# Kernel tuning notes

Measured on AMD Instinct MI355X. Metric: run time of the kernel, lower is better.

## Reference

```python
import jax, jax.numpy as jnp
import numpy as np

N_NODES = 50000
N_EDGES = 300000
HEADS = 2
OUT_CH = 128
BN_EPS = 1e-5
NEG_SLOPE = 0.2


def _batchnorm(x, g, b):
    # training-mode BatchNorm1d: biased batch statistics
    mean = x.mean(axis=0)
    var = x.var(axis=0)
    return (x - mean) * jax.lax.rsqrt(var + BN_EPS) * g + b


def _gatv2(x, src, dst, edge_attr, Wl, bl, Wr, br, We, att, bias, concat):
    # PyG GATv2Conv, share_weights=False, aggr='add'
    n = x.shape[0]
    xl = (x @ Wl + bl).reshape(n, HEADS, OUT_CH)  # source messages
    xr = (x @ Wr + br).reshape(n, HEADS, OUT_CH)  # destination term
    ee = (edge_attr @ We).reshape(-1, HEADS, OUT_CH)
    s = jax.nn.leaky_relu(xl[src] + xr[dst] + ee, NEG_SLOPE)  # [E,H,C]
    alpha = jnp.einsum('ehc,hc->eh', s, att)  # [E,H]
    # segment softmax over edges grouped by destination node
    m = jax.ops.segment_max(alpha, dst, num_segments=n)
    a = jnp.exp(alpha - m[dst])
    den = jax.ops.segment_sum(a, dst, num_segments=n)
    a = a / (den[dst] + 1e-16)
    out = jax.ops.segment_sum(xl[src] * a[:, :, None], dst, num_segments=n)  # [N,H,C]
    out = out.reshape(n, HEADS * OUT_CH) if concat else out.mean(axis=1)
    return out + bias


def setup_inputs() -> dict:
    key = jax.random.key(0)
    ks = jax.random.split(key, 16)
    d = {}
    d['h'] = jax.random.normal(ks[0], (N_NODES, 5), jnp.float32)
    d['edge_index'] = jax.random.randint(ks[1], (2, N_EDGES), 0, N_NODES, jnp.int64)
    d['edge_weight'] = jax.random.uniform(ks[2], (N_EDGES, 1), jnp.float32)
    d['bn0_g'] = jnp.ones((5,), jnp.float32)
    d['bn0_b'] = jnp.zeros((5,), jnp.float32)
    d['bn1_g'] = jnp.ones((256,), jnp.float32)
    d['bn1_b'] = jnp.zeros((256,), jnp.float32)
    def lin(k, fan_in, fan_out):
        return jax.random.normal(k, (fan_in, fan_out), jnp.float32) * (1.0 / np.sqrt(fan_in))
    # conv1: in=5 -> heads*out=256, concat=True
    d['c1_Wl'] = lin(ks[3], 5, 256); d['c1_bl'] = jnp.zeros((256,), jnp.float32)
    d['c1_Wr'] = lin(ks[4], 5, 256); d['c1_br'] = jnp.zeros((256,), jnp.float32)
    d['c1_We'] = lin(ks[5], 1, 256)
    d['c1_att'] = jax.random.normal(ks[6], (HEADS, OUT_CH), jnp.float32) * 0.1
    d['c1_bias'] = jnp.zeros((256,), jnp.float32)
    # mu: in=256 -> 128, concat=False
    d['mu_Wl'] = lin(ks[7], 256, 256); d['mu_bl'] = jnp.zeros((256,), jnp.float32)
    d['mu_Wr'] = lin(ks[8], 256, 256); d['mu_br'] = jnp.zeros((256,), jnp.float32)
    d['mu_We'] = lin(ks[9], 1, 256)
    d['mu_att'] = jax.random.normal(ks[10], (HEADS, OUT_CH), jnp.float32) * 0.1
    d['mu_bias'] = jnp.zeros((128,), jnp.float32)
    # log_std: same shapes as mu
    d['ls_Wl'] = lin(ks[11], 256, 256); d['ls_bl'] = jnp.zeros((256,), jnp.float32)
    d['ls_Wr'] = lin(ks[12], 256, 256); d['ls_br'] = jnp.zeros((256,), jnp.float32)
    d['ls_We'] = lin(ks[13], 1, 256)
    d['ls_att'] = jax.random.normal(ks[14], (HEADS, OUT_CH), jnp.float32) * 0.1
    d['ls_bias'] = jnp.zeros((128,), jnp.float32)
    return d


def reference(h, edge_index, edge_weight, bn0_g, bn0_b, bn1_g, bn1_b,
              c1_Wl, c1_bl, c1_Wr, c1_br, c1_We, c1_att, c1_bias,
              mu_Wl, mu_bl, mu_Wr, mu_br, mu_We, mu_att, mu_bias,
              ls_Wl, ls_bl, ls_Wr, ls_br, ls_We, ls_att, ls_bias):
    src, dst = edge_index[0], edge_index[1]
    x = _batchnorm(h, bn0_g, bn0_b)
    x = _gatv2(x, src, dst, edge_weight, c1_Wl, c1_bl, c1_Wr, c1_br, c1_We, c1_att, c1_bias, concat=True)
    x = jax.nn.relu(_batchnorm(x, bn1_g, bn1_b))
    # dropout identity (eval / deterministic)
    mu = _gatv2(x, src, dst, edge_weight, mu_Wl, mu_bl, mu_Wr, mu_br, mu_We, mu_att, mu_bias, concat=False)
    log_std = _gatv2(x, src, dst, edge_weight, ls_Wl, ls_bl, ls_Wr, ls_br, ls_We, ls_att, ls_bias, concat=False)
    return (mu, log_std)
```

## Files before the change

### kernel.cpp

```cpp
#include <hip/hip_runtime.h>
#include <math.h>

#define N_NODES 50000
#define N_EDGES 300000
#define BN_EPS 1e-5f
#define NEG_SLOPE 0.2f

#define RB_COUNT 3128
#define SCAN_TILES 49
#define BN1_BLOCKS 523
#define K5_BLOCKS 1024

#define AGG_BLOCKS 2048
#define AGG_STRIDE (AGG_BLOCKS * 4)

#define PREP_BN0 128
#define PREP_EC  1172
#define PREP_PW  128

typedef short bf8v __attribute__((ext_vector_type(8)));
typedef float f4v __attribute__((ext_vector_type(4)));
typedef float f2v __attribute__((ext_vector_type(2)));

__device__ inline unsigned short f2bf(float f) {
    union { float f; unsigned u; } c; c.f = f;
    unsigned r = c.u + 0x7fffu + ((c.u >> 16) & 1u);
    return (unsigned short)(r >> 16);
}

__device__ inline unsigned f2bf2(float lo, float hi) {
    return (unsigned)f2bf(lo) | ((unsigned)f2bf(hi) << 16);
}

__device__ inline f2v bfpair(unsigned u) {
    union { unsigned u; float f; } lo, hi;
    lo.u = u << 16;
    hi.u = u & 0xffff0000u;
    f2v r; r.x = lo.f; r.y = hi.f;
    return r;
}

__device__ inline void async_copy16(void* lds, const void* g) {
    __builtin_amdgcn_global_load_lds(
        (const __attribute__((address_space(1))) unsigned int*)g,
        (__attribute__((address_space(3))) unsigned int*)lds, 16, 0, 0);
}

__global__ __launch_bounds__(256) void prep(
        const float* __restrict__ h, float* __restrict__ acc,
        const int* __restrict__ dst, int* __restrict__ count,
        const float* __restrict__ Wl0, const float* __restrict__ Wr0,
        const float* __restrict__ Wl1, const float* __restrict__ Wr1,
        unsigned short* __restrict__ bp) {
    int b = blockIdx.x;
    if (b < PREP_BN0) {
        __shared__ float lds[4][10];
        int tid = threadIdx.x;
        int lane = tid & 63, wave = tid >> 6;
        float ls[5] = {0,0,0,0,0}, lq[5] = {0,0,0,0,0};
        for (int r = b * 256 + tid; r < N_NODES; r += PREP_BN0 * 256) {
            #pragma unroll
            for (int k = 0; k < 5; k++) {
                float v = h[r*5 + k];
                ls[k] += v; lq[k] += v*v;
            }
        }
        #pragma unroll
        for (int k = 0; k < 5; k++) {
            #pragma unroll
            for (int m = 1; m <= 32; m <<= 1) {
                ls[k] += __shfl_xor(ls[k], m, 64);
                lq[k] += __shfl_xor(lq[k], m, 64);
            }
        }
        if (lane == 0) {
            #pragma unroll
            for (int k = 0; k < 5; k++) { lds[wave][k] = ls[k]; lds[wave][5+k] = lq[k]; }
        }
        __syncthreads();
        if (tid < 10) {
            float s = lds[0][tid] + lds[1][tid] + lds[2][tid] + lds[3][tid];
            atomicAdd(&acc[tid], s);
        }
    } else if (b < PREP_BN0 + PREP_EC) {
        int e = (b - PREP_BN0) * 256 + threadIdx.x;
        if (e < N_EDGES) atomicAdd(&count[dst[e]], 1);
    } else {
        int t = (b - PREP_BN0 - PREP_EC) * 256 + threadIdx.x;
        int lane = t & 63;
        int nt = (t >> 6) & 31;
        int kc = (t >> 11) & 7;
        int conv = t >> 14;
        int col = nt * 16 + (lane & 15);
        int k0 = kc * 32 + (lane >> 4) * 8;
        const float* W = conv ? (col < 256 ? Wl1 : Wr1) : (col < 256 ? Wl0 : Wr0);
        int c = col & 255;
        union { unsigned short h[8]; uint4 u; } tmp;
        #pragma unroll
        for (int j = 0; j < 8; j++) tmp.h[j] = f2bf(W[(size_t)(k0 + j) * 256 + c]);
        *reinterpret_cast<uint4*>(bp + (size_t)t * 8) = tmp.u;
    }
}

__global__ void local_scan(const int* __restrict__ count, int* __restrict__ offsets,
                           int* __restrict__ tileSum) {
    __shared__ int wsum[16];
    int tid = threadIdx.x;
    int lane = tid & 63, wv = tid >> 6;
    int i = blockIdx.x * 1024 + tid;
    int v = (i < N_NODES) ? count[i] : 0;
    int inc = v;
    #pragma unroll
    for (int off = 1; off < 64; off <<= 1) {
        int t = __shfl_up(inc, off, 64);
        if (lane >= off) inc += t;
    }
    if (lane == 63) wsum[wv] = inc;
    __syncthreads();
    if (wv == 0) {
        int val = (lane < 16) ? wsum[lane] : 0;
        int inc2 = val;
        #pragma unroll
        for (int off = 1; off < 16; off <<= 1) {
            int t = __shfl_up(inc2, off, 64);
            if (lane >= off) inc2 += t;
        }
        if (lane < 16) wsum[lane] = inc2 - val;
    }
    __syncthreads();
    int excl = inc - v + wsum[wv];
    if (i < N_NODES) offsets[i] = excl;
    if (tid == 1023) tileSum[blockIdx.x] = excl + v;
}

__global__ void add_prefix(int* __restrict__ offsets, const int* __restrict__ tileSum,
                           int* __restrict__ cursor) {
    __shared__ int spref;
    int tid = threadIdx.x;
    if (tid < 64) {
        int v = (tid < blockIdx.x) ? tileSum[tid] : 0;
        #pragma unroll
        for (int m = 1; m <= 32; m <<= 1) v += __shfl_xor(v, m, 64);
        if (tid == 0) spref = v;
    }
    __syncthreads();
    int i = blockIdx.x * 1024 + tid;
    if (i < N_NODES) {
        int o = offsets[i] + spref;
        offsets[i] = o;
        cursor[i] = o;
    }
    if (blockIdx.x == 0 && tid == 0) offsets[N_NODES] = N_EDGES;
}

__global__ void edge_scatter(const int* __restrict__ dst, const int* __restrict__ src,
                             const float* __restrict__ ew, int* __restrict__ cursor,
                             int2* __restrict__ sep) {
    int e = blockIdx.x * blockDim.x + threadIdx.x;
    if (e < N_EDGES) {
        int pos = atomicAdd(&cursor[dst[e]], 1);
        sep[pos] = make_int2(src[e], __float_as_int(ew[e]));
    }
}

__global__ __launch_bounds__(128) void gemm_k5(const float* __restrict__ h,
        const float* __restrict__ acc10, const float* __restrict__ g5,
        const float* __restrict__ b5,
        const float* __restrict__ Wl, const float* __restrict__ bl,
        const float* __restrict__ Wr, const float* __restrict__ br,
        unsigned short* __restrict__ xl, unsigned short* __restrict__ xr) {
    int c = threadIdx.x * 2;
    float sc[5], sh[5];
    #pragma unroll
    for (int k = 0; k < 5; k++) {
        float mean = acc10[k] * (1.f / N_NODES);
        float var  = acc10[5 + k] * (1.f / N_NODES) - mean * mean;
        float s = g5[k] * rsqrtf(var + BN_EPS);
        sc[k] = s; sh[k] = b5[k] - mean * s;
    }
    float wl0[5], wl1[5], wr0[5], wr1[5];
    #pragma unroll
    for (int k = 0; k < 5; k++) {
        wl0[k] = Wl[k*256 + c]; wl1[k] = Wl[k*256 + c + 1];
        wr0[k] = Wr[k*256 + c]; wr1[k] = Wr[k*256 + c + 1];
    }
    float bl0 = bl[c], bl1 = bl[c+1], br0 = br[c], br1 = br[c+1];
    int n = blockIdx.x;
    float hv[5];
    if (n < N_NODES) {
        #pragma unroll
        for (int k = 0; k < 5; k++) hv[k] = h[n*5 + k];
    }
    for (; n < N_NODES; n += K5_BLOCKS) {
        int n2 = n + K5_BLOCKS;
        float hn[5] = {0,0,0,0,0};
        if (n2 < N_NODES) {
            #pragma unroll
            for (int k = 0; k < 5; k++) hn[k] = h[n2*5 + k];
        }
        float l0 = bl0, l1 = bl1, r0 = br0, r1 = br1;
        #pragma unroll
        for (int k = 0; k < 5; k++) {
            float a = hv[k] * sc[k] + sh[k];
            l0 += a * wl0[k]; l1 += a * wl1[k];
            r0 += a * wr0[k]; r1 += a * wr1[k];
        }
        *reinterpret_cast<unsigned*>(xl + (size_t)n*256 + c) = f2bf2(l0, l1);
        *reinterpret_cast<unsigned*>(xr + (size_t)n*256 + c) = f2bf2(r0, r1);
        #pragma unroll
        for (int k = 0; k < 5; k++) hv[k] = hn[k];
    }
}

__global__ __launch_bounds__(256) void gemm_mfma(const unsigned short* __restrict__ xh,
        const float* __restrict__ ss1,
        const unsigned short* __restrict__ bp,
        const float* __restrict__ bl0, const float* __restrict__ br0,
        const float* __restrict__ bl1, const float* __restrict__ br1,
        unsigned short* __restrict__ xlA, unsigned short* __restrict__ xrA,
        unsigned short* __restrict__ xlB, unsigned short* __restrict__ xrB) {
    __shared__ unsigned short Bs[2][16][512];
    int b = blockIdx.x;
    int cv = b >= 1564; b -= cv * 1564;
    int h  = b >= 782;  b -= h * 782;
    int lane = threadIdx.x & 63;
    int wave = threadIdx.x >> 6;
    int rb = b * 4 + wave;

    const unsigned short* bsrc = bp + (size_t)cv * 131072 + (size_t)h * 8192 + lane * 8;
    auto stage = [&](int buf, int kc) {
        #pragma unroll
        for (int j = 0; j < 4; j++) {
            int f = wave * 4 + j;
            async_copy16(&Bs[buf][f][lane * 8], bsrc + (size_t)kc * 16384 + f * 512);
        }
    };
    stage(0, 0);

    int row = rb * 16 + (lane & 15);
    int k0b = (lane >> 4) * 8;
    bool rok = row < N_NODES;
    bf8v a[8];
    #pragma unroll
    for (int kc = 0; kc < 8; kc++) {
        int k0 = kc * 32 + k0b;
        union { unsigned short hh[8]; uint4 u; bf8v v; } tmp;
        if (rok) {
            uint4 u = *(const uint4*)(xh + (size_t)row * 256 + k0);
            f4v s0 = *(const f4v*)(ss1 + k0);
            f4v s1 = *(const f4v*)(ss1 + k0 + 4);
            f4v h0 = *(const f4v*)(ss1 + 256 + k0);
            f4v h1 = *(const f4v*)(ss1 + 256 + k0 + 4);
            float f[8];
            f2v p;
            p = bfpair(u.x); f[0] = p.x; f[1] = p.y;
            p = bfpair(u.y); f[2] = p.x; f[3] = p.y;
            p = bfpair(u.z); f[4] = p.x; f[5] = p.y;
            p = bfpair(u.w); f[6] = p.x; f[7] = p.y;
            float scv[8] = {s0.x, s0.y, s0.z, s0.w, s1.x, s1.y, s1.z, s1.w};
            float shv[8] = {h0.x, h0.y, h0.z, h0.w, h1.x, h1.y, h1.z, h1.w};
            #pragma unroll
            for (int j = 0; j < 8; j++) {
                float v = f[j] * scv[j] + shv[j];
                v = v > 0.f ? v : 0.f;
                tmp.hh[j] = f2bf(v);
            }
        } else {
            tmp.u = (uint4){0u, 0u, 0u, 0u};
        }
        a[kc] = tmp.v;
    }

    f4v acc[16];
    #pragma unroll
    for (int t = 0; t < 16; t++) acc[t] = (f4v){0.f, 0.f, 0.f, 0.f};

    for (int kc = 0; kc < 8; kc++) {
        __syncthreads();
        if (kc < 7) stage((kc + 1) & 1, kc + 1);
        const unsigned short* bb2 = &Bs[kc & 1][0][lane * 8];
        #pragma unroll
        for (int t = 0; t < 16; t++) {
            bf8v bfr = *reinterpret_cast<const bf8v*>(bb2 + t * 512);
            acc[t] = __builtin_amdgcn_mfma_f32_16x16x32_bf16(bfr, a[kc], acc[t], 0, 0, 0);
        }
    }

    int q = lane >> 4;
    unsigned short* outp = cv ? (h ? xrB : xlB) : (h ? xrA : xlA);
    const float* bias = cv ? (h ? br1 : bl1) : (h ? br0 : bl0);
    if (rok) {
        unsigned short* orow = outp + (size_t)row * 256 + q * 4;
        #pragma unroll
        for (int t = 0; t < 16; t++) {
            f4v bv = *(const f4v*)(bias + t * 16 + q * 4);
            uint2 u;
            u.x = f2bf2(acc[t][0] + bv.x, acc[t][1] + bv.y);
            u.y = f2bf2(acc[t][2] + bv.z, acc[t][3] + bv.w);
            *reinterpret_cast<uint2*>(orow + t * 16) = u;
        }
    }
}

__global__ __launch_bounds__(256) void agg_concat(
        const unsigned short* __restrict__ xl, const unsigned short* __restrict__ xr,
        const float* __restrict__ We, const float* __restrict__ att,
        const int* __restrict__ offsets, const int2* __restrict__ sep,
        const float* __restrict__ bias,
        unsigned short* __restrict__ outh) {
    int gw = blockIdx.x * 4 + (threadIdx.x >> 6);
    int lane = threadIdx.x & 63;
    int half = lane >> 5;
    int sub  = lane & 31;
    int cb   = (sub >> 4) * 128 + (sub & 15) * 8;
    f2v wv[4], av[4];
    {
        f4v t0 = *(const f4v*)(We + cb);
        f4v t1 = *(const f4v*)(We + cb + 4);
        wv[0] = (f2v){t0.x, t0.y}; wv[1] = (f2v){t0.z, t0.w};
        wv[2] = (f2v){t1.x, t1.y}; wv[3] = (f2v){t1.z, t1.w};
        t0 = *(const f4v*)(att + cb);
        t1 = *(const f4v*)(att + cb + 4);
        av[0] = (f2v){t0.x, t0.y}; av[1] = (f2v){t0.z, t0.w};
        av[2] = (f2v){t1.x, t1.y}; av[3] = (f2v){t1.z, t1.w};
    }
    int n = gw;
    int beg = 0, end = 0;
    if (n < N_NODES) { beg = offsets[n]; end = offsets[n + 1]; }
    while (n < N_NODES) {
        int nn = n + AGG_STRIDE;
        int nbeg = 0, nend = 0;
        if (nn < N_NODES) { nbeg = offsets[nn]; nend = offsets[nn + 1]; }
        uint4 r8 = *(const uint4*)(xr + ((size_t)n << 8) + cb);
        f2v rv[4];
        rv[0] = bfpair(r8.x); rv[1] = bfpair(r8.y);
        rv[2] = bfpair(r8.z); rv[3] = bfpair(r8.w);

        float den = 0.f;
        f2v acc[4];
        #pragma unroll
        for (int j = 0; j < 4; j++) acc[j] = (f2v){0.f, 0.f};

        int i = beg + half;
        float wN = 0.f;
        int2 seP = make_int2(0, 0);
        uint4 lN = {0u, 0u, 0u, 0u};
        if (i < end) {
            int2 se = sep[i];
            wN = __int_as_float(se.y);
            lN = *(const uint4*)(xl + ((size_t)se.x << 8) + cb);
        }
        if (i + 2 < end) seP = sep[i + 2];
        for (; i < end; i += 2) {
            uint4 l8 = lN; float w = wN;
            if (i + 2 < end) {
                lN = *(const uint4*)(xl + ((size_t)seP.x << 8) + cb);
                wN = __int_as_float(seP.y);
            }
            if (i + 4 < end) seP = sep[i + 4];
            f2v w2 = (f2v){w, w};
            f2v lv[4];
            lv[0] = bfpair(l8.x); lv[1] = bfpair(l8.y);
            lv[2] = bfpair(l8.z); lv[3] = bfpair(l8.w);
            f2v da = (f2v){0.f, 0.f};
            #pragma unroll
            for (int j = 0; j < 4; j++) {
                f2v v = lv[j] + rv[j] + w2 * wv[j];
                f2v s = v * (f2v){NEG_SLOPE, NEG_SLOPE};
                v.x = fmaxf(v.x, s.x); v.y = fmaxf(v.y, s.y);
                da += v * av[j];
            }
            float a = da.x + da.y;
            a += __shfl_xor(a, 1, 64);
            a += __shfl_xor(a, 2, 64);
            a += __shfl_xor(a, 4, 64);
            a += __shfl_xor(a, 8, 64);
            float p = __expf(a);
            den += p;
            f2v p2 = (f2v){p, p};
            #pragma unroll
            for (int j = 0; j < 4; j++) acc[j] += p2 * lv[j];
        }
        den += __shfl_xor(den, 32, 64);
        #pragma unroll
        for (int j = 0; j < 4; j++) {
            f2v ao;
            ao.x = __shfl_xor(acc[j].x, 32, 64);
            ao.y = __shfl_xor(acc[j].y, 32, 64);
            acc[j] += ao;
        }
        float inv = 1.f / (den + 1e-16f);
        if (lane < 32) {
            f4v b0 = *(const f4v*)(bias + cb);
            f4v b1 = *(const f4v*)(bias + cb + 4);
            union { unsigned short hh[8]; uint4 u; } o;
            o.hh[0] = f2bf(acc[0].x * inv + b0.x);
            o.hh[1] = f2bf(acc[0].y * inv + b0.y);
            o.hh[2] = f2bf(acc[1].x * inv + b0.z);
            o.hh[3] = f2bf(acc[1].y * inv + b0.w);
            o.hh[4] = f2bf(acc[2].x * inv + b1.x);
            o.hh[5] = f2bf(acc[2].y * inv + b1.y);
            o.hh[6] = f2bf(acc[3].x * inv + b1.z);
            o.hh[7] = f2bf(acc[3].y * inv + b1.w);
            *(uint4*)(outh + (size_t)n * 256 + cb) = o.u;
        }
        n = nn; beg = nbeg; end = nend;
    }
}

__global__ __launch_bounds__(256) void agg_dual(
        const unsigned short* __restrict__ xlA, const unsigned short* __restrict__ xrA,
        const unsigned short* __restrict__ xlB, const unsigned short* __restrict__ xrB,
        const float* __restrict__ WeA, const float* __restrict__ attA,
        const float* __restrict__ WeB, const float* __restrict__ attB,
        const int* __restrict__ offsets, const int2* __restrict__ sep,
        const float* __restrict__ biasA, const float* __restrict__ biasB,
        float* __restrict__ outA, float* __restrict__ outB) {
    int gw = blockIdx.x * 4 + (threadIdx.x >> 6);
    int lane = threadIdx.x & 63;
    int sub  = lane & 31;
    int cb   = (sub >> 4) * 128 + (sub & 15) * 8;
    int c0   = (lane & 15) * 8;
    int convB = lane >> 5;
    const unsigned short* xlp = (convB ? xlB : xlA) + cb;
    const unsigned short* xrp = (convB ? xrB : xrA) + cb;
    const float* Wep  = convB ? WeB : WeA;
    const float* attp = convB ? attB : attA;
    f2v wv[4], av[4];
    {
        f4v t0 = *(const f4v*)(Wep + cb);
        f4v t1 = *(const f4v*)(Wep + cb + 4);
        wv[0] = (f2v){t0.x, t0.y}; wv[1] = (f2v){t0.z, t0.w};
        wv[2] = (f2v){t1.x, t1.y}; wv[3] = (f2v){t1.z, t1.w};
        t0 = *(const f4v*)(attp + cb);
        t1 = *(const f4v*)(attp + cb + 4);
        av[0] = (f2v){t0.x, t0.y}; av[1] = (f2v){t0.z, t0.w};
        av[2] = (f2v){t1.x, t1.y}; av[3] = (f2v){t1.z, t1.w};
    }
    int n = gw;
    int beg = 0, end = 0;
    if (n < N_NODES) { beg = offsets[n]; end = offsets[n + 1]; }
    while (n < N_NODES) {
        int nn = n + AGG_STRIDE;
        int nbeg = 0, nend = 0;
        if (nn < N_NODES) { nbeg = offsets[nn]; nend = offsets[nn + 1]; }
        uint4 r8 = *(const uint4*)(xrp + ((size_t)n << 8));
        f2v rv[4];
        rv[0] = bfpair(r8.x); rv[1] = bfpair(r8.y);
        rv[2] = bfpair(r8.z); rv[3] = bfpair(r8.w);

        float den = 0.f;
        f2v acc[4];
        #pragma unroll
        for (int j = 0; j < 4; j++) acc[j] = (f2v){0.f, 0.f};

        int i = beg;
        float wN = 0.f, wP = 0.f;
        int sP = 0;
        uint4 lN = {0u, 0u, 0u, 0u};
        if (i < end) {
            int2 se = sep[i];
            wN = __int_as_float(se.y);
            lN = *(const uint4*)(xlp + ((size_t)se.x << 8));
        }
        if (i + 1 < end) { int2 se = sep[i + 1]; sP = se.x; wP = __int_as_float(se.y); }
        for (; i < end; ++i) {
            uint4 l8 = lN; float w = wN;
            if (i + 1 < end) {
                lN = *(const uint4*)(xlp + ((size_t)sP << 8));
                wN = wP;
            }
            if (i + 2 < end) { int2 se = sep[i + 2]; sP = se.x; wP = __int_as_float(se.y); }
            f2v w2 = (f2v){w, w};
            f2v lv[4];
            lv[0] = bfpair(l8.x); lv[1] = bfpair(l8.y);
            lv[2] = bfpair(l8.z); lv[3] = bfpair(l8.w);
            f2v da = (f2v){0.f, 0.f};
            #pragma unroll
            for (int j = 0; j < 4; j++) {
                f2v v = lv[j] + rv[j] + w2 * wv[j];
                f2v s = v * (f2v){NEG_SLOPE, NEG_SLOPE};
                v.x = fmaxf(v.x, s.x); v.y = fmaxf(v.y, s.y);
                da += v * av[j];
            }
            float a = da.x + da.y;
            a += __shfl_xor(a, 1, 64);
            a += __shfl_xor(a, 2, 64);
            a += __shfl_xor(a, 4, 64);
            a += __shfl_xor(a, 8, 64);
            float p = __expf(a);
            den += p;
            f2v p2 = (f2v){p, p};
            #pragma unroll
            for (int j = 0; j < 4; j++) acc[j] += p2 * lv[j];
        }
        float inv = 1.f / (den + 1e-16f);
        float o[8], po[8];
        #pragma unroll
        for (int j = 0; j < 4; j++) {
            o[2*j]   = acc[j].x * inv;
            o[2*j+1] = acc[j].y * inv;
        }
        #pragma unroll
        for (int j = 0; j < 8; j++) po[j] = __shfl_xor(o[j], 16, 64);
        int q = lane >> 4;
        if (q == 0) {
            f4v b0 = *(const f4v*)(biasA + c0);
            f4v b1 = *(const f4v*)(biasA + c0 + 4);
            float r[8];
            r[0] = (o[0]+po[0])*0.5f + b0.x; r[1] = (o[1]+po[1])*0.5f + b0.y;
            r[2] = (o[2]+po[2])*0.5f + b0.z; r[3] = (o[3]+po[3])*0.5f + b0.w;
            r[4] = (o[4]+po[4])*0.5f + b1.x; r[5] = (o[5]+po[5])*0.5f + b1.y;
            r[6] = (o[6]+po[6])*0.5f + b1.z; r[7] = (o[7]+po[7])*0.5f + b1.w;
            *(float4*)(outA + (size_t)n * 128 + c0)     = *(float4*)&r[0];
            *(float4*)(outA + (size_t)n * 128 + c0 + 4) = *(float4*)&r[4];
        } else if (q == 2) {
            f4v b0 = *(const f4v*)(biasB + c0);
            f4v b1 = *(const f4v*)(biasB + c0 + 4);
            float r[8];
            r[0] = (o[0]+po[0])*0.5f + b0.x; r[1] = (o[1]+po[1])*0.5f + b0.y;
            r[2] = (o[2]+po[2])*0.5f + b0.z; r[3] = (o[3]+po[3])*0.5f + b0.w;
            r[4] = (o[4]+po[4])*0.5f + b1.x; r[5] = (o[5]+po[5])*0.5f + b1.y;
            r[6] = (o[6]+po[6])*0.5f + b1.z; r[7] = (o[7]+po[7])*0.5f + b1.w;
            *(float4*)(outB + (size_t)n * 128 + c0)     = *(float4*)&r[0];
            *(float4*)(outB + (size_t)n * 128 + c0 + 4) = *(float4*)&r[4];
        }
        n = nn; beg = nbeg; end = nend;
    }
}

__global__ void bn1_reduce(const unsigned short* __restrict__ xh, float* __restrict__ part) {
    __shared__ float lds[256][9];
    int tid = threadIdx.x;
    int cg = tid & 63;
    int ph = tid >> 6;
    int r0 = blockIdx.x * 96;
    float s[4] = {0,0,0,0}, q[4] = {0,0,0,0};
    #pragma unroll
    for (int it = 0; it < 24; it++) {
        int row = r0 + it * 4 + ph;
        if (row < N_NODES) {
            uint2 v = *(const uint2*)(xh + (size_t)row * 256 + cg * 4);
            f2v p0 = bfpair(v.x), p1 = bfpair(v.y);
            s[0] += p0.x; s[1] += p0.y; s[2] += p1.x; s[3] += p1.y;
            q[0] += p0.x*p0.x; q[1] += p0.y*p0.y; q[2] += p1.x*p1.x; q[3] += p1.y*p1.y;
        }
    }
    #pragma unroll
    for (int j = 0; j < 4; j++) { lds[tid][j] = s[j]; lds[tid][4+j] = q[j]; }
    __syncthreads();
    if (tid < 64) {
        float4 sv, qv;
        float* svp = (float*)&sv; float* qvp = (float*)&qv;
        #pragma unroll
        for (int j = 0; j < 4; j++) {
            svp[j] = lds[tid][j] + lds[tid+64][j] + lds[tid+128][j] + lds[tid+192][j];
            qvp[j] = lds[tid][4+j] + lds[tid+64][4+j] + lds[tid+128][4+j] + lds[tid+192][4+j];
        }
        *(float4*)(part + (size_t)blockIdx.x * 512 + cg * 4) = sv;
        *(float4*)(part + (size_t)blockIdx.x * 512 + 256 + cg * 4) = qv;
    }
}

__global__ void bn1_finalize(const float* __restrict__ part, const float* __restrict__ g,
                             const float* __restrict__ b, float* __restrict__ ss1) {
    __shared__ float lds[8][64];
    int t = threadIdx.x;
    int c = blockIdx.x * 32 + (t & 31);
    int ph = t >> 5;
    float s = 0.f, q = 0.f;
    for (int bi = ph; bi < BN1_BLOCKS; bi += 8) {
        s += part[(size_t)bi * 512 + c];
        q += part[(size_t)bi * 512 + 256 + c];
    }
    lds[ph][t & 31] = s;
    lds[ph][32 + (t & 31)] = q;
    __syncthreads();
    if (t < 32) {
        float ss = 0.f, qq = 0.f;
        #pragma unroll
        for (int p = 0; p < 8; p++) { ss += lds[p][t]; qq += lds[p][32 + t]; }
        float mean = ss * (1.f / N_NODES);
        float var  = qq * (1.f / N_NODES) - mean * mean;
        float sc = g[c] * rsqrtf(var + BN_EPS);
        ss1[c] = sc;
        ss1[256 + c] = b[c] - mean * sc;
    }
}

extern "C" void kernel_launch(void* const* d_in, const int* in_sizes, int n_in,
                              void* d_out, int out_size, void* d_ws, size_t ws_size,
                              hipStream_t stream) {
    const float* h          = (const float*)d_in[0];
    const int*   edge_index = (const int*)d_in[1];
    const int*   src = edge_index;
    const int*   dst = edge_index + N_EDGES;
    const float* ew   = (const float*)d_in[2];
    const float* bn0g = (const float*)d_in[3];
    const float* bn0b = (const float*)d_in[4];
    const float* bn1g = (const float*)d_in[5];
    const float* bn1b = (const float*)d_in[6];
    const float* c1_Wl = (const float*)d_in[7];
    const float* c1_bl = (const float*)d_in[8];
    const float* c1_Wr = (const float*)d_in[9];
    const float* c1_br = (const float*)d_in[10];
    const float* c1_We = (const float*)d_in[11];
    const float* c1_att = (const float*)d_in[12];
    const float* c1_bias = (const float*)d_in[13];
    const float* mu_Wl = (const float*)d_in[14];
    const float* mu_bl = (const float*)d_in[15];
    const float* mu_Wr = (const float*)d_in[16];
    const float* mu_br = (const float*)d_in[17];
    const float* mu_We = (const float*)d_in[18];
    const float* mu_att = (const float*)d_in[19];
    const float* mu_bias = (const float*)d_in[20];
    const float* ls_Wl = (const float*)d_in[21];
    const float* ls_bl = (const float*)d_in[22];
    const float* ls_Wr = (const float*)d_in[23];
    const float* ls_br = (const float*)d_in[24];
    const float* ls_We = (const float*)d_in[25];
    const float* ls_att = (const float*)d_in[26];
    const float* ls_bias = (const float*)d_in[27];

    float* out_mu = (float*)d_out;
    float* out_ls = (float*)d_out + (size_t)N_NODES * 128;

    char* ws = (char*)d_ws;
    size_t off = 0;
    auto alloc = [&](size_t bytes) -> void* {
        void* p = ws + off;
        off += (bytes + 255) / 256 * 256;
        return p;
    };
    unsigned short* xl  = (unsigned short*)alloc((size_t)N_NODES * 256 * 2);
    unsigned short* xr  = (unsigned short*)alloc((size_t)N_NODES * 256 * 2);
    unsigned short* xBh = (unsigned short*)alloc((size_t)N_NODES * 256 * 2);
    unsigned short* xl2 = (unsigned short*)alloc((size_t)N_NODES * 256 * 2);
    unsigned short* xr2 = (unsigned short*)alloc((size_t)N_NODES * 256 * 2);
    float* bn0acc  = (float*)alloc(10 * 4);
    float* bn1part = (float*)alloc((size_t)BN1_BLOCKS * 512 * 4);
    float* bn1ss   = (float*)alloc(512 * 4);
    int*   count   = (int*)alloc((size_t)N_NODES * 4);
    int*   offsets = (int*)alloc((size_t)(N_NODES + 1) * 4);
    int*   cursor  = (int*)alloc((size_t)N_NODES * 4);
    int2*  sep     = (int2*)alloc((size_t)N_EDGES * 8);
    int*   tileSum = (int*)alloc((size_t)SCAN_TILES * 4);
    unsigned short* Bpack = (unsigned short*)alloc((size_t)2 * 131072 * 2);

    hipMemsetAsync(count, 0, (size_t)N_NODES * 4, stream);
    hipMemsetAsync(bn0acc, 0, 10 * 4, stream);

    prep<<<PREP_BN0 + PREP_EC + PREP_PW, 256, 0, stream>>>(
        h, bn0acc, dst, count, mu_Wl, mu_Wr, ls_Wl, ls_Wr, Bpack);

    local_scan<<<SCAN_TILES, 1024, 0, stream>>>(count, offsets, tileSum);
    add_prefix<<<SCAN_TILES, 1024, 0, stream>>>(offsets, tileSum, cursor);
    edge_scatter<<<(N_EDGES + 255) / 256, 256, 0, stream>>>(dst, src, ew, cursor, sep);

    gemm_k5<<<K5_BLOCKS, 128, 0, stream>>>(h, bn0acc, bn0g, bn0b,
                                           c1_Wl, c1_bl, c1_Wr, c1_br, xl, xr);
    agg_concat<<<AGG_BLOCKS, 256, 0, stream>>>(xl, xr, c1_We, c1_att, offsets,
                                               sep, c1_bias, xBh);

    bn1_reduce<<<BN1_BLOCKS, 256, 0, stream>>>(xBh, bn1part);
    bn1_finalize<<<8, 256, 0, stream>>>(bn1part, bn1g, bn1b, bn1ss);

    gemm_mfma<<<3128, 256, 0, stream>>>(xBh, bn1ss, Bpack,
                                        mu_bl, mu_br, ls_bl, ls_br,
                                        xl, xr, xl2, xr2);

    agg_dual<<<AGG_BLOCKS, 256, 0, stream>>>(xl, xr, xl2, xr2,
                                             mu_We, mu_att, ls_We, ls_att,
                                             offsets, sep,
                                             mu_bias, ls_bias, out_mu, out_ls);
}
```

Before: 418.9 us.

## Make MFMA GEMM persistent with full weight tile resident in LDS

The GEMM kernel moves from 3128 small blocks that each re-stage a weight slice through double-buffered LDS to 256 persistent 512-thread blocks. Each block loads its full 256x256-column weight slice (128 KB) into shared memory once, then loops over 49 row-blocks. This removes per-block weight re-staging and the barriers inside the k loop. In exchange, the large LDS footprint limits occupancy to one block per CU, and 256 blocks with an uneven tail may leave some CUs underused.

```diff
diff --git a/kernel.cpp b/kernel.cpp
--- a/kernel.cpp
+++ b/kernel.cpp
@@ -17,6 +17,8 @@
 #define PREP_BN0 128
 #define PREP_EC  1172
 #define PREP_PW  128
+
+#define GEMM_RB_PER_G 49
 
 typedef short bf8v __attribute__((ext_vector_type(8)));
 typedef float f4v __attribute__((ext_vector_type(4)));
@@ -212,92 +214,97 @@
     }
 }
 
-__global__ __launch_bounds__(256) void gemm_mfma(const unsigned short* __restrict__ xh,
+__global__ __launch_bounds__(512) void gemm_mfma(const unsigned short* __restrict__ xh,
         const float* __restrict__ ss1,
         const unsigned short* __restrict__ bp,
         const float* __restrict__ bl0, const float* __restrict__ br0,
         const float* __restrict__ bl1, const float* __restrict__ br1,
         unsigned short* __restrict__ xlA, unsigned short* __restrict__ xrA,
         unsigned short* __restrict__ xlB, unsigned short* __restrict__ xrB) {
-    __shared__ unsigned short Bs[2][16][512];
+    __shared__ unsigned short Bs[8][16][512];
     int b = blockIdx.x;
-    int cv = b >= 1564; b -= cv * 1564;
-    int h  = b >= 782;  b -= h * 782;
+    int cv = b & 1;
+    int h  = (b >> 1) & 1;
+    int g  = b >> 2;
     int lane = threadIdx.x & 63;
     int wave = threadIdx.x >> 6;
-    int rb = b * 4 + wave;
-
-    const unsigned short* bsrc = bp + (size_t)cv * 131072 + (size_t)h * 8192 + lane * 8;
-    auto stage = [&](int buf, int kc) {
-        #pragma unroll
-        for (int j = 0; j < 4; j++) {
-            int f = wave * 4 + j;
-            async_copy16(&Bs[buf][f][lane * 8], bsrc + (size_t)kc * 16384 + f * 512);
-        }
-    };
-    stage(0, 0);
-
-    int row = rb * 16 + (lane & 15);
-    int k0b = (lane >> 4) * 8;
-    bool rok = row < N_NODES;
-    bf8v a[8];
-    #pragma unroll
-    for (int kc = 0; kc < 8; kc++) {
-        int k0 = kc * 32 + k0b;
-        union { unsigned short hh[8]; uint4 u; bf8v v; } tmp;
-        if (rok) {
-            uint4 u = *(const uint4*)(xh + (size_t)row * 256 + k0);
-            f4v s0 = *(const f4v*)(ss1 + k0);
-            f4v s1 = *(const f4v*)(ss1 + k0 + 4);
-            f4v h0 = *(const f4v*)(ss1 + 256 + k0);
-            f4v h1 = *(const f4v*)(ss1 + 256 + k0 + 4);
-            float f[8];
-            f2v p;
-            p = bfpair(u.x); f[0] = p.x; f[1] = p.y;
-            p = bfpair(u.y); f[2] = p.x; f[3] = p.y;
-            p = bfpair(u.z); f[4] = p.x; f[5] = p.y;
-            p = bfpair(u.w); f[6] = p.x; f[7] = p.y;
-            float scv[8] = {s0.x, s0.y, s0.z, s0.w, s1.x, s1.y, s1.z, s1.w};
-            float shv[8] = {h0.x, h0.y, h0.z, h0.w, h1.x, h1.y, h1.z, h1.w};
-            #pragma unroll
-            for (int j = 0; j < 8; j++) {
-                float v = f[j] * scv[j] + shv[j];
-                v = v > 0.f ? v : 0.f;
-                tmp.hh[j] = f2bf(v);
-            }
-        } else {
-            tmp.u = (uint4){0u, 0u, 0u, 0u};
-        }
-        a[kc] = tmp.v;
-    }
-
-    f4v acc[16];
-    #pragma unroll
-    for (int t = 0; t < 16; t++) acc[t] = (f4v){0.f, 0.f, 0.f, 0.f};
-
-    for (int kc = 0; kc < 8; kc++) {
-        __syncthreads();
-        if (kc < 7) stage((kc + 1) & 1, kc + 1);
-        const unsigned short* bb2 = &Bs[kc & 1][0][lane * 8];
-        #pragma unroll
-        for (int t = 0; t < 16; t++) {
-            bf8v bfr = *reinterpret_cast<const bf8v*>(bb2 + t * 512);
-            acc[t] = __builtin_amdgcn_mfma_f32_16x16x32_bf16(bfr, a[kc], acc[t], 0, 0, 0);
-        }
-    }
+
+    {
+        const unsigned short* bsrc = bp + (size_t)cv * 131072 + (size_t)h * 8192
+                                        + (size_t)wave * 16384 + lane * 8;
+        #pragma unroll
+        for (int f = 0; f < 16; f++) {
+            async_copy16(&Bs[wave][f][lane * 8], bsrc + f * 512);
+        }
+    }
+    __syncthreads();
 
     int q = lane >> 4;
+    int k0b = q * 8;
     unsigned short* outp = cv ? (h ? xrB : xlB) : (h ? xrA : xlA);
     const float* bias = cv ? (h ? br1 : bl1) : (h ? br0 : bl0);
-    if (rok) {
-        unsigned short* orow = outp + (size_t)row * 256 + q * 4;
-        #pragma unroll
-        for (int t = 0; t < 16; t++) {
-            f4v bv = *(const f4v*)(bias + t * 16 + q * 4);
-            uint2 u;
-            u.x = f2bf2(acc[t][0] + bv.x, acc[t][1] + bv.y);
-            u.y = f2bf2(acc[t][2] + bv.z, acc[t][3] + bv.w);
-            *reinterpret_cast<uint2*>(orow + t * 16) = u;
+    int rbEnd = (g + 1) * GEMM_RB_PER_G;
+    if (rbEnd > RB_COUNT) rbEnd = RB_COUNT;
+
+    for (int rb = g * GEMM_RB_PER_G + wave; rb < rbEnd; rb += 8) {
+        int row = rb * 16 + (lane & 15);
+        bool rok = row < N_NODES;
+
+        bf8v a[8];
+        #pragma unroll
+        for (int kc = 0; kc < 8; kc++) {
+            int k0 = kc * 32 + k0b;
+            union { unsigned short hh[8]; uint4 u; bf8v v; } tmp;
+            if (rok) {
+                uint4 u = *(const uint4*)(xh + (size_t)row * 256 + k0);
+                f4v s0 = *(const f4v*)(ss1 + k0);
+                f4v s1 = *(const f4v*)(ss1 + k0 + 4);
+                f4v h0 = *(const f4v*)(ss1 + 256 + k0);
+                f4v h1 = *(const f4v*)(ss1 + 256 + k0 + 4);
+                float f[8];
+                f2v p;
+                p = bfpair(u.x); f[0] = p.x; f[1] = p.y;
+                p = bfpair(u.y); f[2] = p.x; f[3] = p.y;
+                p = bfpair(u.z); f[4] = p.x; f[5] = p.y;
+                p = bfpair(u.w); f[6] = p.x; f[7] = p.y;
+                float scv[8] = {s0.x, s0.y, s0.z, s0.w, s1.x, s1.y, s1.z, s1.w};
+                float shv[8] = {h0.x, h0.y, h0.z, h0.w, h1.x, h1.y, h1.z, h1.w};
+                #pragma unroll
+                for (int j = 0; j < 8; j++) {
+                    float v = f[j] * scv[j] + shv[j];
+                    v = v > 0.f ? v : 0.f;
+                    tmp.hh[j] = f2bf(v);
+                }
+            } else {
+                tmp.u = (uint4){0u, 0u, 0u, 0u};
+            }
+            a[kc] = tmp.v;
+        }
+
+        f4v acc[16];
+        #pragma unroll
+        for (int t = 0; t < 16; t++) acc[t] = (f4v){0.f, 0.f, 0.f, 0.f};
+
+        #pragma unroll
+        for (int kc = 0; kc < 8; kc++) {
+            const unsigned short* bb2 = &Bs[kc][0][lane * 8];
+            #pragma unroll
+            for (int t = 0; t < 16; t++) {
+                bf8v bfr = *reinterpret_cast<const bf8v*>(bb2 + t * 512);
+                acc[t] = __builtin_amdgcn_mfma_f32_16x16x32_bf16(bfr, a[kc], acc[t], 0, 0, 0);
+            }
+        }
+
+        if (rok) {
+            unsigned short* orow = outp + (size_t)row * 256 + q * 4;
+            #pragma unroll
+            for (int t = 0; t < 16; t++) {
+                f4v bv = *(const f4v*)(bias + t * 16 + q * 4);
+                uint2 u;
+                u.x = f2bf2(acc[t][0] + bv.x, acc[t][1] + bv.y);
+                u.y = f2bf2(acc[t][2] + bv.z, acc[t][3] + bv.w);
+                *reinterpret_cast<uint2*>(orow + t * 16) = u;
+            }
         }
     }
 }
@@ -665,9 +672,9 @@
     bn1_reduce<<<BN1_BLOCKS, 256, 0, stream>>>(xBh, bn1part);
     bn1_finalize<<<8, 256, 0, stream>>>(bn1part, bn1g, bn1b, bn1ss);
 
-    gemm_mfma<<<3128, 256, 0, stream>>>(xBh, bn1ss, Bpack,
-                                        mu_bl, mu_br, ls_bl, ls_br,
-                                        xl, xr, xl2, xr2);
+    gemm_mfma<<<256, 512, 0, stream>>>(xBh, bn1ss, Bpack,
+                                       mu_bl, mu_br, ls_bl, ls_br,
+                                       xl, xr, xl2, xr2);
 
     agg_dual<<<AGG_BLOCKS, 256, 0, stream>>>(xl, xr, xl2, xr2,
                                              mu_We, mu_att, ls_We, ls_att,
```

New measurement: 763.7 us. 1.82x slower.
